# Optimization experiments

Measured on AMD Instinct MI355X. Metric: run time of the kernel, lower is better.

The kernel has to match this reference:

```python
import jax, jax.numpy as jnp
import numpy as np

EMB = 512
HEAD = 64
B, S = 4, 4096


def setup_inputs() -> dict:
    key = jax.random.key(0)
    kq, kk, kv, kwq, kwk, kwv = jax.random.split(key, 6)
    q = jax.random.normal(kq, (B, S, EMB), dtype=jnp.float32)
    k = jax.random.normal(kk, (B, S, EMB), dtype=jnp.float32)
    v = jax.random.normal(kv, (B, S, EMB), dtype=jnp.float32)
    # nn.Linear weights: [out_features, in_features], no bias
    sc = 1.0 / np.sqrt(EMB)
    Wq = jax.random.uniform(kwq, (HEAD, EMB), jnp.float32, -sc, sc)
    Wk = jax.random.uniform(kwk, (HEAD, EMB), jnp.float32, -sc, sc)
    Wv = jax.random.uniform(kwv, (HEAD, EMB), jnp.float32, -sc, sc)
    return {"q": q, "k": k, "v": v, "Wq": Wq, "Wk": Wk, "Wv": Wv}


def reference(q, k, v, Wq, Wk, Wv):
    scale = 1.0 / np.sqrt(HEAD).astype(np.float32)
    Q = jnp.einsum('bse,he->bsh', q, Wq)  # [B,S,HEAD]
    K = jnp.einsum('bse,he->bsh', k, Wk)
    V = jnp.einsum('bse,he->bsh', v, Wv)
    scores = jnp.einsum('bqh,bkh->bqk', Q, K) * scale  # [B,S,S]
    attn = jax.nn.softmax(scores, axis=-1)
    # dropout p=0.0 -> identity
    out = jnp.einsum('bqk,bkh->bqh', attn, V)  # [B,S,HEAD]
    return out
```

## Files before the change

### kernel.cpp

```cpp
#include <hip/hip_runtime.h>
#include <hip/hip_bf16.h>

#define EMB    512
#define HEAD   64
#define SEQ    4096
#define NB     4
#define NSPLIT 4
#define LDX    72

typedef __bf16 bf16x8 __attribute__((ext_vector_type(8)));
typedef float  f32x4  __attribute__((ext_vector_type(4)));

__device__ inline ushort4 cvt4(float4 v) {
    __hip_bfloat16 a = __float2bfloat16(v.x), b = __float2bfloat16(v.y);
    __hip_bfloat16 c = __float2bfloat16(v.z), d = __float2bfloat16(v.w);
    ushort4 r;
    r.x = *(unsigned short*)&a; r.y = *(unsigned short*)&b;
    r.z = *(unsigned short*)&c; r.w = *(unsigned short*)&d;
    return r;
}

__global__ __launch_bounds__(256) void proj_kernel(
    const float* __restrict__ q, const float* __restrict__ k, const float* __restrict__ v,
    const float* __restrict__ Wq, const float* __restrict__ Wk, const float* __restrict__ Wv,
    __hip_bfloat16* __restrict__ Qo, __hip_bfloat16* __restrict__ Ko,
    __hip_bfloat16* __restrict__ Vto)
{
    __shared__ __hip_bfloat16 Xs[64][LDX];
    __shared__ __hip_bfloat16 Ws[64][LDX];

    const int which = blockIdx.y;
    const float* __restrict__ x = (which == 0) ? q : (which == 1) ? k : v;
    const float* __restrict__ W = (which == 0) ? Wq : (which == 1) ? Wk : Wv;

    const int tid  = threadIdx.x;
    const int wave = tid >> 6, lane = tid & 63;
    const int l16  = lane & 15, quad = lane >> 4;
    const int r0   = blockIdx.x * 64;

    const f32x4 z = {0.f, 0.f, 0.f, 0.f};
    f32x4 acc[4] = {z, z, z, z};

    for (int e0 = 0; e0 < EMB; e0 += 64) {
        if (e0) __syncthreads();
        #pragma unroll
        for (int it = 0; it < 4; ++it) {
            int idx = it * 256 + tid;
            int r = idx >> 4, c4 = (idx & 15) << 2;
            float4 xv = *(const float4*)(x + (size_t)(r0 + r) * EMB + e0 + c4);
            *(ushort4*)&Xs[r][c4] = cvt4(xv);
            float4 wv = *(const float4*)(W + (size_t)r * EMB + e0 + c4);
            *(ushort4*)&Ws[r][c4] = cvt4(wv);
        }
        __syncthreads();

        #pragma unroll
        for (int st = 0; st < 2; ++st) {
            bf16x8 a = *(const bf16x8*)&Xs[wave * 16 + l16][st * 32 + quad * 8];
            #pragma unroll
            for (int t = 0; t < 4; ++t) {
                bf16x8 b = *(const bf16x8*)&Ws[t * 16 + l16][st * 32 + quad * 8];
                acc[t] = __builtin_amdgcn_mfma_f32_16x16x32_bf16(a, b, acc[t], 0, 0, 0);
            }
        }
    }

    #pragma unroll
    for (int t = 0; t < 4; ++t) {
        #pragma unroll
        for (int r = 0; r < 4; ++r) {
            int row = r0 + wave * 16 + quad * 4 + r;
            int h   = t * 16 + l16;
            __hip_bfloat16 val = __float2bfloat16(acc[t][r]);
            if (which == 0) {
                Qo[(size_t)row * HEAD + h] = val;
            } else if (which == 1) {
                Ko[(size_t)row * HEAD + h] = val;
            } else {
                int b = row >> 12, s = row & (SEQ - 1);
                Vto[((size_t)b * HEAD + h) * SEQ + s] = val;
            }
        }
    }
}

__global__ __launch_bounds__(256) void attn_kernel(
    const __hip_bfloat16* __restrict__ Qb, const __hip_bfloat16* __restrict__ Kb,
    const __hip_bfloat16* __restrict__ Vt, float* __restrict__ Op,
    float* __restrict__ lp)
{
    __shared__ __hip_bfloat16 QPs[64][LDX];
    __shared__ __hip_bfloat16 Ks[64][LDX];
    __shared__ __hip_bfloat16 Vs[64][LDX];

    const int tid  = threadIdx.x;
    const int wave = tid >> 6, lane = tid & 63;
    const int l16  = lane & 15, quad = lane >> 4;
    const int b    = blockIdx.y;
    const int q0   = blockIdx.x * 64;
    const int split = blockIdx.z;
    const int j0base = split * (SEQ / NSPLIT);

    for (int i = tid; i < 512; i += 256) {
        int r = i >> 3, c8 = (i & 7) * 8;
        *(uint4*)&QPs[r][c8] =
            *(const uint4*)(Qb + ((size_t)b * SEQ + q0 + r) * HEAD + c8);
    }
    __syncthreads();

    bf16x8 qf0 = *(const bf16x8*)&QPs[wave * 16 + l16][quad * 8];
    bf16x8 qf1 = *(const bf16x8*)&QPs[wave * 16 + l16][32 + quad * 8];

    const f32x4 z = {0.f, 0.f, 0.f, 0.f};
    f32x4 oacc[4] = {z, z, z, z};
    float l_r[4] = {0.f, 0.f, 0.f, 0.f};

    const float sl2e = 0.18033688011112042f;

    for (int jt = 0; jt < SEQ / NSPLIT; jt += 64) {
        const int j0 = j0base + jt;
        __syncthreads();
        for (int i = tid; i < 512; i += 256) {
            int r = i >> 3, c8 = (i & 7) * 8;
            *(uint4*)&Ks[r][c8] =
                *(const uint4*)(Kb + ((size_t)b * SEQ + j0 + r) * HEAD + c8);
            *(uint4*)&Vs[r][c8] =
                *(const uint4*)(Vt + ((size_t)b * HEAD + r) * SEQ + j0 + c8);
        }
        __syncthreads();

        f32x4 sacc[4] = {z, z, z, z};
        #pragma unroll
        for (int st = 0; st < 2; ++st) {
            bf16x8 a = (st == 0) ? qf0 : qf1;
            #pragma unroll
            for (int t = 0; t < 4; ++t) {
                bf16x8 bK = *(const bf16x8*)&Ks[t * 16 + l16][st * 32 + quad * 8];
                sacc[t] = __builtin_amdgcn_mfma_f32_16x16x32_bf16(a, bK, sacc[t], 0, 0, 0);
            }
        }

        #pragma unroll
        for (int r = 0; r < 4; ++r) {
            float ls = 0.f;
            #pragma unroll
            for (int t = 0; t < 4; ++t) {
                float p = __builtin_amdgcn_exp2f(sacc[t][r] * sl2e);
                ls += p;
                QPs[wave * 16 + quad * 4 + r][t * 16 + l16] = __float2bfloat16(p);
            }
            l_r[r] += ls;
        }

        #pragma unroll
        for (int st = 0; st < 2; ++st) {
            bf16x8 pf = *(const bf16x8*)&QPs[wave * 16 + l16][st * 32 + quad * 8];
            #pragma unroll
            for (int t = 0; t < 4; ++t) {
                bf16x8 vf = *(const bf16x8*)&Vs[t * 16 + l16][st * 32 + quad * 8];
                oacc[t] = __builtin_amdgcn_mfma_f32_16x16x32_bf16(pf, vf, oacc[t], 0, 0, 0);
            }
        }
    }

    #pragma unroll
    for (int r = 0; r < 4; ++r) {
        float s = l_r[r];
        #pragma unroll
        for (int off = 1; off < 16; off <<= 1) s += __shfl_xor(s, off);
        l_r[r] = s;
    }
    const size_t pb = (size_t)(split * NB + b) * SEQ;
    if (l16 == 0) {
        #pragma unroll
        for (int r = 0; r < 4; ++r)
            lp[pb + q0 + wave * 16 + quad * 4 + r] = l_r[r];
    }
    #pragma unroll
    for (int t = 0; t < 4; ++t)
        #pragma unroll
        for (int r = 0; r < 4; ++r)
            Op[(pb + q0 + wave * 16 + quad * 4 + r) * HEAD + t * 16 + l16] = oacc[t][r];
}

__global__ __launch_bounds__(256) void merge_kernel(
    const float* __restrict__ Op, const float* __restrict__ lp,
    float* __restrict__ out)
{
    int idx = blockIdx.x * 256 + threadIdx.x;
    int bq  = idx >> 4;
    int c4  = (idx & 15) * 4;
    float4 acc = {0.f, 0.f, 0.f, 0.f};
    float  l   = 0.f;
    #pragma unroll
    for (int s = 0; s < NSPLIT; ++s) {
        float4 o = *(const float4*)(Op + ((size_t)s * NB * SEQ + bq) * HEAD + c4);
        acc.x += o.x; acc.y += o.y; acc.z += o.z; acc.w += o.w;
        l += lp[(size_t)s * NB * SEQ + bq];
    }
    float inv = 1.f / l;
    float4 r = {acc.x * inv, acc.y * inv, acc.z * inv, acc.w * inv};
    *(float4*)(out + (size_t)bq * HEAD + c4) = r;
}

extern "C" void kernel_launch(void* const* d_in, const int* in_sizes, int n_in,
                              void* d_out, int out_size, void* d_ws, size_t ws_size,
                              hipStream_t stream) {
    const float* q  = (const float*)d_in[0];
    const float* k  = (const float*)d_in[1];
    const float* v  = (const float*)d_in[2];
    const float* Wq = (const float*)d_in[3];
    const float* Wk = (const float*)d_in[4];
    const float* Wv = (const float*)d_in[5];
    float* out = (float*)d_out;

    __hip_bfloat16* Qb = (__hip_bfloat16*)d_ws;
    __hip_bfloat16* Kb = Qb + (size_t)NB * SEQ * HEAD;
    __hip_bfloat16* Vt = Kb + (size_t)NB * SEQ * HEAD;
    float* Op = (float*)(Vt + (size_t)NB * SEQ * HEAD);
    float* lp = Op + (size_t)NSPLIT * NB * SEQ * HEAD;

    dim3 pgrid(NB * SEQ / 64, 3);
    proj_kernel<<<pgrid, dim3(256), 0, stream>>>(q, k, v, Wq, Wk, Wv, Qb, Kb, Vt);

    dim3 agrid(SEQ / 64, NB, NSPLIT);
    attn_kernel<<<agrid, dim3(256), 0, stream>>>(Qb, Kb, Vt, Op, lp);

    merge_kernel<<<(NB * SEQ * 16) / 256, dim3(256), 0, stream>>>(Op, lp, out);
}
```

Baseline: 190.2 us.

## Prefetch tiles in registers, pre-convert weights, and merge attention splits with atomics

The weights are converted to bf16 once in a separate kernel, with the softmax scale times log2(e) folded into Wq. The projection kernel then reads W fragments straight from global memory. Both the projection and attention kernels now prefetch the next X or K/V tile into registers while the current tile computes. The KV split count goes from 4 to 8, and partial outputs are accumulated with atomicAdd into a zeroed buffer, which lets the merge become a simple normalize pass. Launch-bounds occupancy hints are added as well. The price is atomic contention, an extra memset and kernel launch, and float accumulation whose order is nondeterministic.

```diff
diff --git a/kernel.cpp b/kernel.cpp
--- a/kernel.cpp
+++ b/kernel.cpp
@@ -5,8 +5,10 @@
 #define HEAD   64
 #define SEQ    4096
 #define NB     4
-#define NSPLIT 4
+#define NSPLIT 8
 #define LDX    72
+
+#define SL2E   0.18033688011112042f
 
 typedef __bf16 bf16x8 __attribute__((ext_vector_type(8)));
 typedef float  f32x4  __attribute__((ext_vector_type(4)));
@@ -20,50 +22,95 @@
     return r;
 }
 
-__global__ __launch_bounds__(256) void proj_kernel(
+__global__ __launch_bounds__(256) void cvtw_kernel(
+    const float* __restrict__ Wq, const float* __restrict__ Wk,
+    const float* __restrict__ Wv, __hip_bfloat16* __restrict__ Wc)
+{
+    int idx   = blockIdx.x * 256 + threadIdx.x;
+    int which = idx >> 13;
+    int off   = (idx & 8191) * 4;
+    const float* src = (which == 0) ? Wq : (which == 1) ? Wk : Wv;
+    float s = (which == 0) ? SL2E : 1.0f;
+    float4 v = *(const float4*)(src + off);
+    v.x *= s; v.y *= s; v.z *= s; v.w *= s;
+    *(ushort4*)(Wc + which * 64 * EMB + off) = cvt4(v);
+}
+
+__global__ __launch_bounds__(256, 3) void proj_kernel(
     const float* __restrict__ q, const float* __restrict__ k, const float* __restrict__ v,
-    const float* __restrict__ Wq, const float* __restrict__ Wk, const float* __restrict__ Wv,
+    const __hip_bfloat16* __restrict__ Wc,
     __hip_bfloat16* __restrict__ Qo, __hip_bfloat16* __restrict__ Ko,
     __hip_bfloat16* __restrict__ Vto)
 {
     __shared__ __hip_bfloat16 Xs[64][LDX];
-    __shared__ __hip_bfloat16 Ws[64][LDX];
 
     const int which = blockIdx.y;
     const float* __restrict__ x = (which == 0) ? q : (which == 1) ? k : v;
-    const float* __restrict__ W = (which == 0) ? Wq : (which == 1) ? Wk : Wv;
+    const __hip_bfloat16* __restrict__ W = Wc + which * 64 * EMB;
 
     const int tid  = threadIdx.x;
     const int wave = tid >> 6, lane = tid & 63;
     const int l16  = lane & 15, quad = lane >> 4;
     const int r0   = blockIdx.x * 64;
+    const float* __restrict__ xb = x + (size_t)r0 * EMB;
+
+    const int sr = tid >> 4;
+    const int sc = (tid & 15) << 2;
 
     const f32x4 z = {0.f, 0.f, 0.f, 0.f};
     f32x4 acc[4] = {z, z, z, z};
 
-    for (int e0 = 0; e0 < EMB; e0 += 64) {
-        if (e0) __syncthreads();
-        #pragma unroll
-        for (int it = 0; it < 4; ++it) {
-            int idx = it * 256 + tid;
-            int r = idx >> 4, c4 = (idx & 15) << 2;
-            float4 xv = *(const float4*)(x + (size_t)(r0 + r) * EMB + e0 + c4);
-            *(ushort4*)&Xs[r][c4] = cvt4(xv);
-            float4 wv = *(const float4*)(W + (size_t)r * EMB + e0 + c4);
-            *(ushort4*)&Ws[r][c4] = cvt4(wv);
-        }
+    float4 xr[4];
+    bf16x8 wf[8];
+
+#define LOADX(dst, e0)                                                        \
+    _Pragma("unroll")                                                         \
+    for (int it = 0; it < 4; ++it)                                            \
+        dst[it] = *(const float4*)(xb + (size_t)(it * 16 + sr) * EMB + (e0) + sc);
+
+#define LOADW(dst, e0)                                                        \
+    _Pragma("unroll")                                                         \
+    for (int st = 0; st < 2; ++st)                                            \
+        _Pragma("unroll")                                                     \
+        for (int t = 0; t < 4; ++t)                                           \
+            dst[st * 4 + t] = *(const bf16x8*)(W + (size_t)(t * 16 + l16) * EMB \
+                                               + (e0) + st * 32 + quad * 8);
+
+    LOADX(xr, 0);
+    LOADW(wf, 0);
+
+    #pragma unroll
+    for (int c = 0; c < 8; ++c) {
+        const int e0 = c * 64;
+        if (c) __syncthreads();
+        #pragma unroll
+        for (int it = 0; it < 4; ++it)
+            *(ushort4*)&Xs[it * 16 + sr][sc] = cvt4(xr[it]);
         __syncthreads();
 
-        #pragma unroll
-        for (int st = 0; st < 2; ++st) {
-            bf16x8 a = *(const bf16x8*)&Xs[wave * 16 + l16][st * 32 + quad * 8];
-            #pragma unroll
-            for (int t = 0; t < 4; ++t) {
-                bf16x8 b = *(const bf16x8*)&Ws[t * 16 + l16][st * 32 + quad * 8];
-                acc[t] = __builtin_amdgcn_mfma_f32_16x16x32_bf16(a, b, acc[t], 0, 0, 0);
-            }
-        }
-    }
+        bf16x8 a0 = *(const bf16x8*)&Xs[wave * 16 + l16][quad * 8];
+        bf16x8 a1 = *(const bf16x8*)&Xs[wave * 16 + l16][32 + quad * 8];
+
+        float4 xr2[4];
+        bf16x8 wf2[8];
+        if (c < 7) { LOADX(xr2, e0 + 64); LOADW(wf2, e0 + 64); }
+
+        #pragma unroll
+        for (int t = 0; t < 4; ++t)
+            acc[t] = __builtin_amdgcn_mfma_f32_16x16x32_bf16(a0, wf[t], acc[t], 0, 0, 0);
+        #pragma unroll
+        for (int t = 0; t < 4; ++t)
+            acc[t] = __builtin_amdgcn_mfma_f32_16x16x32_bf16(a1, wf[4 + t], acc[t], 0, 0, 0);
+
+        if (c < 7) {
+            #pragma unroll
+            for (int it = 0; it < 4; ++it) xr[it] = xr2[it];
+            #pragma unroll
+            for (int j = 0; j < 8; ++j) wf[j] = wf2[j];
+        }
+    }
+#undef LOADX
+#undef LOADW
 
     #pragma unroll
     for (int t = 0; t < 4; ++t) {
@@ -84,10 +131,10 @@
     }
 }
 
-__global__ __launch_bounds__(256) void attn_kernel(
+__global__ __launch_bounds__(256, 4) void attn_kernel(
     const __hip_bfloat16* __restrict__ Qb, const __hip_bfloat16* __restrict__ Kb,
-    const __hip_bfloat16* __restrict__ Vt, float* __restrict__ Op,
-    float* __restrict__ lp)
+    const __hip_bfloat16* __restrict__ Vt, float* __restrict__ OG,
+    float* __restrict__ lG)
 {
     __shared__ __hip_bfloat16 QPs[64][LDX];
     __shared__ __hip_bfloat16 Ks[64][LDX];
@@ -98,8 +145,7 @@
     const int l16  = lane & 15, quad = lane >> 4;
     const int b    = blockIdx.y;
     const int q0   = blockIdx.x * 64;
-    const int split = blockIdx.z;
-    const int j0base = split * (SEQ / NSPLIT);
+    const int j0b  = blockIdx.z * (SEQ / NSPLIT);
 
     for (int i = tid; i < 512; i += 256) {
         int r = i >> 3, c8 = (i & 7) * 8;
@@ -115,19 +161,33 @@
     f32x4 oacc[4] = {z, z, z, z};
     float l_r[4] = {0.f, 0.f, 0.f, 0.f};
 
-    const float sl2e = 0.18033688011112042f;
+    uint4 kr[2], vr[2];
+
+#define LOADKV(kd, vd, j0)                                                     \
+    _Pragma("unroll")                                                          \
+    for (int it = 0; it < 2; ++it) {                                           \
+        int i = it * 256 + tid;                                                \
+        int r = i >> 3, c8 = (i & 7) * 8;                                      \
+        kd[it] = *(const uint4*)(Kb + ((size_t)b * SEQ + (j0) + r) * HEAD + c8); \
+        vd[it] = *(const uint4*)(Vt + ((size_t)b * HEAD + r) * SEQ + (j0) + c8); \
+    }
+
+    LOADKV(kr, vr, j0b);
 
     for (int jt = 0; jt < SEQ / NSPLIT; jt += 64) {
-        const int j0 = j0base + jt;
         __syncthreads();
-        for (int i = tid; i < 512; i += 256) {
+        #pragma unroll
+        for (int it = 0; it < 2; ++it) {
+            int i = it * 256 + tid;
             int r = i >> 3, c8 = (i & 7) * 8;
-            *(uint4*)&Ks[r][c8] =
-                *(const uint4*)(Kb + ((size_t)b * SEQ + j0 + r) * HEAD + c8);
-            *(uint4*)&Vs[r][c8] =
-                *(const uint4*)(Vt + ((size_t)b * HEAD + r) * SEQ + j0 + c8);
+            *(uint4*)&Ks[r][c8] = kr[it];
+            *(uint4*)&Vs[r][c8] = vr[it];
         }
         __syncthreads();
+
+        uint4 kr2[2], vr2[2];
+        const bool more = (jt + 64 < SEQ / NSPLIT);
+        if (more) { LOADKV(kr2, vr2, j0b + jt + 64); }
 
         f32x4 sacc[4] = {z, z, z, z};
         #pragma unroll
@@ -145,7 +205,7 @@
             float ls = 0.f;
             #pragma unroll
             for (int t = 0; t < 4; ++t) {
-                float p = __builtin_amdgcn_exp2f(sacc[t][r] * sl2e);
+                float p = __builtin_amdgcn_exp2f(sacc[t][r]);
                 ls += p;
                 QPs[wave * 16 + quad * 4 + r][t * 16 + l16] = __float2bfloat16(p);
             }
@@ -161,7 +221,13 @@
                 oacc[t] = __builtin_amdgcn_mfma_f32_16x16x32_bf16(pf, vf, oacc[t], 0, 0, 0);
             }
         }
-    }
+
+        if (more) {
+            #pragma unroll
+            for (int it = 0; it < 2; ++it) { kr[it] = kr2[it]; vr[it] = vr2[it]; }
+        }
+    }
+#undef LOADKV
 
     #pragma unroll
     for (int r = 0; r < 4; ++r) {
@@ -170,36 +236,28 @@
         for (int off = 1; off < 16; off <<= 1) s += __shfl_xor(s, off);
         l_r[r] = s;
     }
-    const size_t pb = (size_t)(split * NB + b) * SEQ;
+    const size_t row0 = (size_t)b * SEQ + q0 + wave * 16 + quad * 4;
     if (l16 == 0) {
         #pragma unroll
+        for (int r = 0; r < 4; ++r) atomicAdd(&lG[row0 + r], l_r[r]);
+    }
+    #pragma unroll
+    for (int t = 0; t < 4; ++t)
+        #pragma unroll
         for (int r = 0; r < 4; ++r)
-            lp[pb + q0 + wave * 16 + quad * 4 + r] = l_r[r];
-    }
-    #pragma unroll
-    for (int t = 0; t < 4; ++t)
-        #pragma unroll
-        for (int r = 0; r < 4; ++r)
-            Op[(pb + q0 + wave * 16 + quad * 4 + r) * HEAD + t * 16 + l16] = oacc[t][r];
-}
-
-__global__ __launch_bounds__(256) void merge_kernel(
-    const float* __restrict__ Op, const float* __restrict__ lp,
+            atomicAdd(&OG[(row0 + r) * HEAD + t * 16 + l16], oacc[t][r]);
+}
+
+__global__ __launch_bounds__(256) void norm_kernel(
+    const float* __restrict__ OG, const float* __restrict__ lG,
     float* __restrict__ out)
 {
     int idx = blockIdx.x * 256 + threadIdx.x;
     int bq  = idx >> 4;
     int c4  = (idx & 15) * 4;
-    float4 acc = {0.f, 0.f, 0.f, 0.f};
-    float  l   = 0.f;
-    #pragma unroll
-    for (int s = 0; s < NSPLIT; ++s) {
-        float4 o = *(const float4*)(Op + ((size_t)s * NB * SEQ + bq) * HEAD + c4);
-        acc.x += o.x; acc.y += o.y; acc.z += o.z; acc.w += o.w;
-        l += lp[(size_t)s * NB * SEQ + bq];
-    }
-    float inv = 1.f / l;
-    float4 r = {acc.x * inv, acc.y * inv, acc.z * inv, acc.w * inv};
+    float4 o = *(const float4*)(OG + (size_t)bq * HEAD + c4);
+    float inv = 1.f / lG[bq];
+    float4 r = {o.x * inv, o.y * inv, o.z * inv, o.w * inv};
     *(float4*)(out + (size_t)bq * HEAD + c4) = r;
 }
 
@@ -217,14 +275,18 @@
     __hip_bfloat16* Qb = (__hip_bfloat16*)d_ws;
     __hip_bfloat16* Kb = Qb + (size_t)NB * SEQ * HEAD;
     __hip_bfloat16* Vt = Kb + (size_t)NB * SEQ * HEAD;
-    float* Op = (float*)(Vt + (size_t)NB * SEQ * HEAD);
-    float* lp = Op + (size_t)NSPLIT * NB * SEQ * HEAD;
+    __hip_bfloat16* Wc = Vt + (size_t)NB * SEQ * HEAD;
+    float* OG = (float*)(Wc + 3 * 64 * EMB);
+    float* lG = OG + (size_t)NB * SEQ * HEAD;
+
+    cvtw_kernel<<<96, 256, 0, stream>>>(Wq, Wk, Wv, Wc);
+    hipMemsetAsync(OG, 0, (size_t)NB * SEQ * HEAD * 4 + (size_t)NB * SEQ * 4, stream);
 
     dim3 pgrid(NB * SEQ / 64, 3);
-    proj_kernel<<<pgrid, dim3(256), 0, stream>>>(q, k, v, Wq, Wk, Wv, Qb, Kb, Vt);
+    proj_kernel<<<pgrid, dim3(256), 0, stream>>>(q, k, v, Wc, Qb, Kb, Vt);
 
     dim3 agrid(SEQ / 64, NB, NSPLIT);
-    attn_kernel<<<agrid, dim3(256), 0, stream>>>(Qb, Kb, Vt, Op, lp);
-
-    merge_kernel<<<(NB * SEQ * 16) / 256, dim3(256), 0, stream>>>(Op, lp, out);
-}
+    attn_kernel<<<agrid, dim3(256), 0, stream>>>(Qb, Kb, Vt, OG, lG);
+
+    norm_kernel<<<(NB * SEQ * 16) / 256, dim3(256), 0, stream>>>(OG, lG, out);
+}
```

Result: slower. 291.9 us (+53.4%).
